# Kernel optimization log

Hardware: AMD Instinct MI355X
Metric: run time of the kernel (lower is better)

The kernel has to match this reference:

```python
import jax, jax.numpy as jnp
import numpy as np

NUM_USERS = 60000
NUM_ITEMS = 30000
EMBED_K = 64
FEAT_DIM = 64
E_HALF = 1000000
N_LAYERS = 3
LM = 0.5
BATCH = 100000
EPS = 1e-8


def setup_inputs() -> dict:
    key = jax.random.key(0)
    ks = jax.random.split(key, 14)
    Gu = jax.random.normal(ks[0], (NUM_USERS, EMBED_K), jnp.float32) * 0.05
    Gi = jax.random.normal(ks[1], (NUM_ITEMS, EMBED_K), jnp.float32) * 0.05
    Bu = jax.random.normal(ks[2], (NUM_USERS, 1), jnp.float32) * 0.05
    Bi = jax.random.normal(ks[3], (NUM_ITEMS, 1), jnp.float32) * 0.05
    Mu = jax.random.normal(ks[4], (1, 1), jnp.float32) * 0.05
    proj_W = jax.random.normal(ks[5], (FEAT_DIM, EMBED_K), jnp.float32) * 0.05
    proj_b = jnp.zeros((EMBED_K,), jnp.float32)
    gcn_W = jax.random.normal(ks[6], (N_LAYERS, EMBED_K, EMBED_K), jnp.float32) * 0.05
    gcn_b = jnp.zeros((N_LAYERS, EMBED_K), jnp.float32)
    edge_features = jax.random.normal(ks[7], (E_HALF, FEAT_DIM), jnp.float32)
    # first half rows MUST be item-node ids (>= NUM_USERS) since update_adjacency
    # indexes node_embeddings[row[:E//2] - num_users]
    users = jax.random.randint(ks[8], (E_HALF,), 0, NUM_USERS, jnp.int32)
    items = jax.random.randint(ks[9], (E_HALF,), 0, NUM_ITEMS, jnp.int32) + NUM_USERS
    edge_row = jnp.concatenate([items, users], axis=0)
    edge_col = jnp.concatenate([users, items], axis=0)
    L0 = jnp.ones((2 * E_HALF,), jnp.float32)
    user_idx = jax.random.randint(ks[10], (BATCH,), 0, NUM_USERS, jnp.int32)
    item_idx = jax.random.randint(ks[11], (BATCH,), 0, NUM_ITEMS, jnp.int32)
    return {"Gu": Gu, "Gi": Gi, "Bu": Bu, "Bi": Bi, "Mu": Mu,
            "proj_W": proj_W, "proj_b": proj_b, "gcn_W": gcn_W, "gcn_b": gcn_b,
            "edge_features": edge_features, "L0": L0,
            "edge_row": edge_row, "edge_col": edge_col,
            "user_idx": user_idx, "item_idx": item_idx}


def reference(Gu, Gi, Bu, Bi, Mu, proj_W, proj_b, gcn_W, gcn_b,
              edge_features, L0, edge_row, edge_col, user_idx, item_idx):
    num_users = Gu.shape[0]
    N = num_users + Gi.shape[0]
    Eh = edge_features.shape[0]
    row_h = edge_row[:Eh]  # item-node ids for the first (undirected) half
    # projection of edge features is identical every layer -> hoist
    proj = edge_features @ proj_W + proj_b  # [Eh, K]
    x = jnp.concatenate([Gu, Gi], axis=0)  # [N, K]
    for l in range(gcn_W.shape[0]):
        # update_adjacency (aggr='sim'): cosine sim of feature-gated endpoint embeddings
        rn = x[row_h]                       # [Eh, K] gather
        cn = x[row_h - num_users]           # [Eh, K] gather (as in original code)
        a = rn * proj
        b = cn * proj
        na = jnp.maximum(jnp.sqrt(jnp.sum(a * a, -1)), EPS)
        nb = jnp.maximum(jnp.sqrt(jnp.sum(b * b, -1)), EPS)
        sim = jax.nn.relu(jnp.sum(a * b, -1) / (na * nb))
        vals = LM * L0 + (1.0 - LM) * jnp.concatenate([sim, sim], axis=0)  # [E]
        # GCNConv with normalize=True, add_self_loops=False on weighted adjacency
        deg = jax.ops.segment_sum(vals, edge_row, num_segments=N)
        dinv = jnp.where(deg > 0, jax.lax.rsqrt(jnp.where(deg > 0, deg, 1.0)), 0.0)
        ew = dinv[edge_row] * vals * dinv[edge_col]   # [E]
        h = x @ gcn_W[l]                               # [N, K]
        agg = jax.ops.segment_sum(ew[:, None] * h[edge_col], edge_row, num_segments=N)
        x = jax.nn.relu(agg + gcn_b[l])
    gu = x[:num_users]
    gi = x[num_users:]
    # forward/predict: dot-product + biases + global offset
    xui = (jnp.sum(gu[user_idx] * gi[item_idx], axis=1)
           + Bu[user_idx, 0] + Bi[item_idx, 0] + Mu[0, 0])
    return xui
```

## Files before the change

kernel.cpp:

```cpp
#include <hip/hip_runtime.h>
#include <hip/hip_fp16.h>

#define NUSERS 60000
#define NITEMS 30000
#define NNODES 90000
#define KDIM 64
#define EH 1000000
#define E2 2000000
#define NBATCH 100000
#define EPSV 1e-8f

#define NB 128
#define RPB_I 240
#define RPB_U 472
#define CHUNK 2048
#define NPAD_I 32768
#define NPAD_U 61440

typedef __attribute__((ext_vector_type(8))) short short8v;
typedef __attribute__((ext_vector_type(4))) float f32x4;

__device__ inline float4 h4_to_f4(const __half* p) {
    float2 raw = *(const float2*)p;
    __half2 a = *(__half2*)&raw.x;
    __half2 b = *(__half2*)&raw.y;
    float2 fa = __half22float2(a), fb = __half22float2(b);
    return make_float4(fa.x, fa.y, fb.x, fb.y);
}

__global__ void k_count2(const int* __restrict__ erow, const int* __restrict__ ecol,
                         int* __restrict__ cntI, int* __restrict__ cntU) {
    int e = blockIdx.x * 256 + threadIdx.x;
    if (e < EH) {
        atomicAdd(&cntI[erow[e] - NUSERS], 1);
        atomicAdd(&cntU[ecol[e]], 1);
    }
}

__global__ void k_scan2(const int* __restrict__ cntI, int* __restrict__ ofsI,
                        int* __restrict__ curI, const int* __restrict__ cntU,
                        int* __restrict__ ofsU, int* __restrict__ curU) {
    const int* counts; int* offsets; int* cursor; int n;
    if (blockIdx.x == 0) { counts = cntI; offsets = ofsI; cursor = curI; n = NITEMS; }
    else                 { counts = cntU; offsets = ofsU; cursor = curU; n = NUSERS; }
    __shared__ int wsum[17];
    int t = threadIdx.x;
    int lane = t & 63, wid = t >> 6;
    int carry = 0;
    int npad = (n + 4095) & ~4095;
    for (int base = 0; base < npad; base += 4096) {
        int i0 = base + t * 4;
        int4 v = *(const int4*)&counts[i0];
        int s0 = v.x, s1 = s0 + v.y, s2 = s1 + v.z, s3 = s2 + v.w;
        int ws = s3;
#pragma unroll
        for (int o = 1; o < 64; o <<= 1) {
            int u = __shfl_up(ws, o, 64);
            if (lane >= o) ws += u;
        }
        if (lane == 63) wsum[wid] = ws;
        __syncthreads();
        if (wid == 0) {
            int wv = (lane < 16) ? wsum[lane] : 0;
#pragma unroll
            for (int o = 1; o < 16; o <<= 1) {
                int u = __shfl_up(wv, o, 64);
                if (lane >= o) wv += u;
            }
            if (lane < 16) wsum[lane] = wv;
            if (lane == 15) wsum[16] = wv;
        }
        __syncthreads();
        int wbase = (wid > 0) ? wsum[wid - 1] : 0;
        int texcl = carry + wbase + (ws - s3);
        if (i0 < n)     { offsets[i0]     = texcl;      cursor[i0]     = texcl; }
        if (i0 + 1 < n) { offsets[i0 + 1] = texcl + s0; cursor[i0 + 1] = texcl + s0; }
        if (i0 + 2 < n) { offsets[i0 + 2] = texcl + s1; cursor[i0 + 2] = texcl + s1; }
        if (i0 + 3 < n) { offsets[i0 + 3] = texcl + s2; cursor[i0 + 3] = texcl + s2; }
        carry += wsum[16];
        __syncthreads();
    }
    if (t == 0) offsets[n] = carry;
}

__global__ void k_bcur2(const int* __restrict__ ofsI, const int* __restrict__ ofsU,
                        int* __restrict__ gcurI, int* __restrict__ gcurU) {
    int t = threadIdx.x;
    if (t < NB) {
        int rI = t * RPB_I; if (rI > NITEMS) rI = NITEMS;
        int rU = t * RPB_U; if (rU > NUSERS) rU = NUSERS;
        gcurI[t] = ofsI[rI];
        gcurU[t] = ofsU[rU];
    }
}

template <int PHASE, int RPBX>
__global__ void k_binA(const int* __restrict__ erow, const int* __restrict__ ecol,
                       const int* __restrict__ inv, int* __restrict__ gcur,
                       int* __restrict__ srow, int2* __restrict__ spay) {
    __shared__ int bcnt[NB];
    __shared__ int bbase[NB];
    __shared__ int bpos[NB];
    __shared__ int bglob[NB];
    __shared__ int wtot[2];
    __shared__ int lrow[CHUNK];
    __shared__ int2 lce[CHUNK];
    int t = threadIdx.x;
    for (int base = blockIdx.x * CHUNK; base < EH; base += gridDim.x * CHUNK) {
        for (int i = t; i < NB; i += 256) bcnt[i] = 0;
        __syncthreads();
        int mr[8], mx[8], my[8], mb[8];
#pragma unroll
        for (int k = 0; k < 8; ++k) {
            int e = base + k * 256 + t;
            if (e < EH) {
                int r, px, py;
                if (PHASE == 0) { r = erow[e] - NUSERS; px = ecol[e]; py = e; }
                else            { r = ecol[e];          px = erow[e]; py = inv[e]; }
                mr[k] = r; mx[k] = px; my[k] = py;
                mb[k] = r / RPBX;
                atomicAdd(&bcnt[mb[k]], 1);
            } else {
                mb[k] = -1;
            }
        }
        __syncthreads();
        if (t < NB) {
            int v = bcnt[t];
            int s = v;
#pragma unroll
            for (int o = 1; o < 64; o <<= 1) {
                int u = __shfl_up(s, o, 64);
                if ((t & 63) >= o) s += u;
            }
            bbase[t] = s - v;
            if ((t & 63) == 63) wtot[t >> 6] = s;
        }
        __syncthreads();
        if (t >= 64 && t < NB) bbase[t] += wtot[0];
        if (t < NB) bpos[t] = 0;
        __syncthreads();
#pragma unroll
        for (int k = 0; k < 8; ++k) {
            if (mb[k] >= 0) {
                int p = bbase[mb[k]] + atomicAdd(&bpos[mb[k]], 1);
                lrow[p] = mr[k];
                lce[p] = make_int2(mx[k], my[k]);
            }
        }
        __syncthreads();
        if (t < NB) bglob[t] = bcnt[t] ? atomicAdd(&gcur[t], bcnt[t]) : 0;
        __syncthreads();
        int total = bbase[NB - 1] + bcnt[NB - 1];
        for (int i = t; i < total; i += 256) {
            int r = lrow[i];
            int b = r / RPBX;
            int dest = bglob[b] + (i - bbase[b]);
            srow[dest] = r;
            spay[dest] = lce[i];
        }
        __syncthreads();
    }
}

__global__ void k_binB0(const int* __restrict__ srow, const int2* __restrict__ spay,
                        const int* __restrict__ ofsI, int* __restrict__ curI,
                        const float* __restrict__ L0, int* __restrict__ colp,
                        int* __restrict__ eorig, int* __restrict__ inv,
                        float2* __restrict__ L0p) {
    int b = blockIdx.x;
    int r0 = b * RPB_I; if (r0 > NITEMS) r0 = NITEMS;
    int r1 = (b + 1) * RPB_I; if (r1 > NITEMS) r1 = NITEMS;
    int lo = ofsI[r0], hi = ofsI[r1];
    for (int i = lo + threadIdx.x; i < hi; i += blockDim.x) {
        int r = srow[i];
        int2 p = spay[i];
        int slot = atomicAdd(&curI[r], 1);
        colp[slot] = p.x;
        eorig[slot] = p.y;
        inv[p.y] = slot;
        L0p[slot] = make_float2(L0[p.y], L0[p.y + EH]);
    }
}

__global__ void k_binB1(const int* __restrict__ srow, const int2* __restrict__ spay,
                        const int* __restrict__ ofsU, int* __restrict__ curU,
                        int2* __restrict__ csrU) {
    int b = blockIdx.x;
    int r0 = b * RPB_U; if (r0 > NUSERS) r0 = NUSERS;
    int r1 = (b + 1) * RPB_U; if (r1 > NUSERS) r1 = NUSERS;
    int lo = ofsU[r0], hi = ofsU[r1];
    for (int i = lo + threadIdx.x; i < hi; i += blockDim.x) {
        int r = srow[i];
        int2 p = spay[i];
        int slot = atomicAdd(&curU[r], 1);
        csrU[slot] = p;
    }
}

template <int MODE>
__global__ void k_gemm(const float* __restrict__ A, const float* __restrict__ W,
                       const float* __restrict__ bias, void* __restrict__ out, int M,
                       const int* __restrict__ eorig, __half* __restrict__ xh) {
    __shared__ float Ws[4096];
    int t = threadIdx.x;
    for (int i = t; i < 4096; i += 256) Ws[i] = W[i];
    __syncthreads();
    int lane = t & 63;
    int wid = t >> 6;
    int lr = lane & 15;
    int kg = lane >> 4;
    short8v Bh[2][4], Bl[2][4];
#pragma unroll
    for (int kt = 0; kt < 2; ++kt)
#pragma unroll
        for (int ct = 0; ct < 4; ++ct) {
            short8v bh, bl;
#pragma unroll
            for (int i = 0; i < 8; ++i) {
                int k = kt * 32 + kg * 8 + i;
                float v = Ws[k * 64 + ct * 16 + lr];
                unsigned u = __float_as_uint(v);
                float d = v - __uint_as_float(u & 0xffff0000u);
                bh[i] = (short)(u >> 16);
                bl[i] = (short)(__float_as_uint(d) >> 16);
            }
            Bh[kt][ct] = bh;
            Bl[kt][ct] = bl;
        }
    float bcol[4];
    if (MODE == 1) {
#pragma unroll
        for (int ct = 0; ct < 4; ++ct) bcol[ct] = bias[ct * 16 + lr];
    }
    int nt = M >> 4;
    int nw = gridDim.x * 4;
    for (int tile = blockIdx.x * 4 + wid; tile < nt; tile += nw) {
        int r0 = tile << 4;
        int arow = (MODE == 1) ? eorig[r0 + lr] : (r0 + lr);
        const float* ap = &A[(size_t)arow * 64 + kg * 8];
        float4 a0 = *(const float4*)ap;
        float4 a1 = *(const float4*)(ap + 4);
        float4 a2 = *(const float4*)(ap + 32);
        float4 a3 = *(const float4*)(ap + 36);
        float av[16] = {a0.x, a0.y, a0.z, a0.w, a1.x, a1.y, a1.z, a1.w,
                        a2.x, a2.y, a2.z, a2.w, a3.x, a3.y, a3.z, a3.w};
        if (MODE == 0) {
            short8v pk0, pk1;
#pragma unroll
            for (int i = 0; i < 8; ++i) {
                pk0[i] = __half_as_short(__float2half(av[i]));
                pk1[i] = __half_as_short(__float2half(av[8 + i]));
            }
            *(short8v*)&xh[(size_t)(r0 + lr) * 64 + kg * 8] = pk0;
            *(short8v*)&xh[(size_t)(r0 + lr) * 64 + 32 + kg * 8] = pk1;
        }
        short8v Ah[2], Al[2];
#pragma unroll
        for (int kt = 0; kt < 2; ++kt) {
            short8v ah, al;
#pragma unroll
            for (int i = 0; i < 8; ++i) {
                float v = av[kt * 8 + i];
                unsigned u = __float_as_uint(v);
                float d = v - __uint_as_float(u & 0xffff0000u);
                ah[i] = (short)(u >> 16);
                al[i] = (short)(__float_as_uint(d) >> 16);
            }
            Ah[kt] = ah;
            Al[kt] = al;
        }
        f32x4 acc[4] = {{0, 0, 0, 0}, {0, 0, 0, 0}, {0, 0, 0, 0}, {0, 0, 0, 0}};
#pragma unroll
        for (int kt = 0; kt < 2; ++kt)
#pragma unroll
            for (int ct = 0; ct < 4; ++ct) {
                acc[ct] = __builtin_amdgcn_mfma_f32_16x16x32_bf16(Ah[kt], Bh[kt][ct], acc[ct], 0, 0, 0);
                acc[ct] = __builtin_amdgcn_mfma_f32_16x16x32_bf16(Al[kt], Bh[kt][ct], acc[ct], 0, 0, 0);
                acc[ct] = __builtin_amdgcn_mfma_f32_16x16x32_bf16(Ah[kt], Bl[kt][ct], acc[ct], 0, 0, 0);
            }
#pragma unroll
        for (int ct = 0; ct < 4; ++ct)
#pragma unroll
            for (int r = 0; r < 4; ++r) {
                int row = r0 + kg * 4 + r;
                int col = ct * 16 + lr;
                float p = acc[ct][r];
                if (MODE == 1) {
                    p += bcol[ct];
                    ((__half*)out)[(size_t)row * 64 + col] = __float2half(p * p);
                } else {
                    ((__half*)out)[(size_t)row * 64 + col] = __float2half(p);
                }
            }
    }
}

__global__ void __launch_bounds__(256) k_sim(
        const __half* __restrict__ xh, const __half* __restrict__ qp,
        const int* __restrict__ colp, const float2* __restrict__ L0p,
        const int* __restrict__ ofsI, float* __restrict__ v1p,
        float* __restrict__ v2p, float* __restrict__ deg) {
    int t = threadIdx.x;
    int wid = t >> 6, lane = t & 63, g = lane >> 4, kq = lane & 15;
    int item = blockIdx.x * 4 + wid;
    if (item >= NITEMS) return;
    float4 rn = h4_to_f4(&xh[(size_t)(NUSERS + item) * 64 + kq * 4]);
    int jb = ofsI[item], je = ofsI[item + 1];
    float dacc = 0.0f;
    for (int j0 = jb; j0 < je; j0 += 4) {
        int j = j0 + g;
        bool act = j < je;
        int user = 0;
        float4 cn = make_float4(0, 0, 0, 0), qv = make_float4(0, 0, 0, 0);
        if (act) {
            user = colp[j];
            cn = h4_to_f4(&xh[(size_t)user * 64 + kq * 4]);
            qv = h4_to_f4(&qp[(size_t)j * 64 + kq * 4]);
        }
        float aa = rn.x * rn.x * qv.x + rn.y * rn.y * qv.y + rn.z * rn.z * qv.z + rn.w * rn.w * qv.w;
        float bb = cn.x * cn.x * qv.x + cn.y * cn.y * qv.y + cn.z * cn.z * qv.z + cn.w * cn.w * qv.w;
        float ab = rn.x * cn.x * qv.x + rn.y * cn.y * qv.y + rn.z * cn.z * qv.z + rn.w * cn.w * qv.w;
#pragma unroll
        for (int m = 1; m < 16; m <<= 1) {
            aa += __shfl_xor(aa, m, 64);
            bb += __shfl_xor(bb, m, 64);
            ab += __shfl_xor(ab, m, 64);
        }
        if (kq == 0 && act) {
            float na = fmaxf(sqrtf(aa), EPSV);
            float nb = fmaxf(sqrtf(bb), EPSV);
            float sim = fmaxf(ab / (na * nb), 0.0f);
            float2 l0 = L0p[j];
            float v1 = 0.5f * l0.x + 0.5f * sim;
            float v2 = 0.5f * l0.y + 0.5f * sim;
            v1p[j] = v1;
            v2p[j] = v2;
            atomicAdd(&deg[user], v2);
            dacc += v1;
        }
    }
    dacc += __shfl_xor(dacc, 16, 64);
    dacc += __shfl_xor(dacc, 32, 64);
    if (lane == 0) deg[NUSERS + item] = dacc;
}

__global__ void k_dinv(const float* __restrict__ deg, float* __restrict__ dinv) {
    int n = blockIdx.x * 256 + threadIdx.x;
    if (n < NNODES) {
        float d = deg[n];
        dinv[n] = d > 0.0f ? rsqrtf(d) : 0.0f;
    }
}

#define IBLK 3750
__global__ void __launch_bounds__(256) k_agg(
        const int* __restrict__ ofsI, const int* __restrict__ colp,
        const float* __restrict__ v1p, const int* __restrict__ ofsU,
        const int2* __restrict__ csrU, const float* __restrict__ v2p,
        const float* __restrict__ dinv, const __half* __restrict__ h,
        const float* __restrict__ bias, float* __restrict__ xo) {
    int t = threadIdx.x;
    int half_id = t >> 5, sl = t & 31;
    const __half2* h2 = (const __half2*)h;
    float2 bv = ((const float2*)bias)[sl];
    float2 acc = make_float2(0.0f, 0.0f);
    int node;
    if (blockIdx.x < IBLK) {
        int il = blockIdx.x * 8 + half_id;
        node = NUSERS + il;
        float dn = dinv[node];
        int jb = ofsI[il], je = ofsI[il + 1];
        for (int j0 = jb; j0 < je; j0 += 32) {
            int cnt = je - j0;
            if (cnt > 32) cnt = 32;
            int col = 0;
            float wgt = 0.0f;
            if (sl < cnt) {
                col = colp[j0 + sl];
                wgt = dn * v1p[j0 + sl] * dinv[col];
            }
            for (int u = 0; u < cnt; ++u) {
                int c = __shfl(col, u, 32);
                float wv = __shfl(wgt, u, 32);
                float2 hv = __half22float2(h2[(size_t)c * 32 + sl]);
                acc.x += wv * hv.x;
                acc.y += wv * hv.y;
            }
        }
    } else {
        int ul = (blockIdx.x - IBLK) * 8 + half_id;
        node = ul;
        float dn = dinv[ul];
        int jb = ofsU[ul], je = ofsU[ul + 1];
        for (int j0 = jb; j0 < je; j0 += 32) {
            int cnt = je - j0;
            if (cnt > 32) cnt = 32;
            int col = 0;
            float wgt = 0.0f;
            if (sl < cnt) {
                int2 ce = csrU[j0 + sl];
                col = ce.x;
                wgt = dn * v2p[ce.y] * dinv[col];
            }
            for (int u = 0; u < cnt; ++u) {
                int c = __shfl(col, u, 32);
                float wv = __shfl(wgt, u, 32);
                float2 hv = __half22float2(h2[(size_t)c * 32 + sl]);
                acc.x += wv * hv.x;
                acc.y += wv * hv.y;
            }
        }
    }
    float2 o = make_float2(fmaxf(acc.x + bv.x, 0.0f), fmaxf(acc.y + bv.y, 0.0f));
    ((float2*)xo)[(size_t)node * 32 + sl] = o;
}

__global__ void k_final(const float* __restrict__ x, const int* __restrict__ uidx,
                        const int* __restrict__ iidx, const float* __restrict__ Bu,
                        const float* __restrict__ Bi, const float* __restrict__ Mu,
                        float* __restrict__ out) {
    int t = threadIdx.x;
    int le = t >> 4, kq = t & 15, k0 = kq * 4;
    int i = blockIdx.x * 16 + le;
    if (i >= NBATCH) return;
    int u = uidx[i], it = iidx[i];
    float4 a = *(const float4*)&x[(size_t)u * 64 + k0];
    float4 b = *(const float4*)&x[(size_t)(NUSERS + it) * 64 + k0];
    float d = a.x * b.x + a.y * b.y + a.z * b.z + a.w * b.w;
#pragma unroll
    for (int m = 1; m < 16; m <<= 1) d += __shfl_xor(d, m, 64);
    if (kq == 0) out[i] = d + Bu[u] + Bi[it] + Mu[0];
}

extern "C" void kernel_launch(void* const* d_in, const int* in_sizes, int n_in,
                              void* d_out, int out_size, void* d_ws, size_t ws_size,
                              hipStream_t stream) {
    const float* Gu    = (const float*)d_in[0];
    const float* Gi    = (const float*)d_in[1];
    const float* Bu    = (const float*)d_in[2];
    const float* Bi    = (const float*)d_in[3];
    const float* Mu    = (const float*)d_in[4];
    const float* projW = (const float*)d_in[5];
    const float* projb = (const float*)d_in[6];
    const float* gcnW  = (const float*)d_in[7];
    const float* gcnb  = (const float*)d_in[8];
    const float* ef    = (const float*)d_in[9];
    const float* L0    = (const float*)d_in[10];
    const int*   erow  = (const int*)d_in[11];
    const int*   ecol  = (const int*)d_in[12];
    const int*   uidx  = (const int*)d_in[13];
    const int*   iidx  = (const int*)d_in[14];
    float* out = (float*)d_out;

    char* w = (char*)d_ws;
    size_t off = 0;
    auto take = [&](size_t bytes) -> void* {
        void* p = w + off;
        off += (bytes + 255) & ~(size_t)255;
        return p;
    };
    float*  x0    = (float*)take((size_t)NNODES * KDIM * 4);
    float*  x1    = (float*)take((size_t)NNODES * KDIM * 4);
    __half* h     = (__half*)take((size_t)NNODES * KDIM * 2);
    __half* xh    = (__half*)take((size_t)NNODES * KDIM * 2);
    float*  v1p   = (float*)take((size_t)EH * 4);
    float*  v2p   = (float*)take((size_t)EH * 4);
    float*  deg   = (float*)take((size_t)NNODES * 4);
    float*  dinv  = (float*)take((size_t)NNODES * 4);
    int*    cntI  = (int*)take((size_t)NPAD_I * 4);
    int*    cntU  = (int*)take((size_t)NPAD_U * 4);
    int*    ofsI  = (int*)take((size_t)(NITEMS + 1) * 4);
    int*    curI  = (int*)take((size_t)(NITEMS + 1) * 4);
    int*    ofsU  = (int*)take((size_t)(NUSERS + 1) * 4);
    int*    curU  = (int*)take((size_t)(NUSERS + 1) * 4);
    int*    gcurI = (int*)take((size_t)NB * 4);
    int*    gcurU = (int*)take((size_t)NB * 4);
    int*    colp  = (int*)take((size_t)EH * 4);
    int*    eorig = (int*)take((size_t)EH * 4);
    int*    inv   = (int*)take((size_t)EH * 4);
    float2* L0p   = (float2*)take((size_t)EH * 8);
    int2*   csrU  = (int2*)take((size_t)EH * 8);
    __half* qp    = (__half*)take((size_t)EH * KDIM * 2);
    int*  srow = (int*)qp;
    int2* spay = (int2*)((char*)qp + (size_t)EH * 4);

    hipMemsetAsync(cntI, 0, (size_t)(NPAD_I + NPAD_U) * 4, stream);
    k_count2<<<(EH + 255) / 256, 256, 0, stream>>>(erow, ecol, cntI, cntU);
    k_scan2<<<2, 1024, 0, stream>>>(cntI, ofsI, curI, cntU, ofsU, curU);
    k_bcur2<<<1, 128, 0, stream>>>(ofsI, ofsU, gcurI, gcurU);
    k_binA<0, RPB_I><<<256, 256, 0, stream>>>(erow, ecol, nullptr, gcurI, srow, spay);
    k_binB0<<<NB, 512, 0, stream>>>(srow, spay, ofsI, curI, L0, colp, eorig, inv, L0p);
    k_binA<1, RPB_U><<<256, 256, 0, stream>>>(erow, ecol, inv, gcurU, srow, spay);
    k_binB1<<<NB, 512, 0, stream>>>(srow, spay, ofsU, curU, csrU);

    k_gemm<1><<<1024, 256, 0, stream>>>(ef, projW, projb, qp, EH, eorig, nullptr);

    hipMemcpyAsync(x0, Gu, (size_t)NUSERS * KDIM * 4, hipMemcpyDeviceToDevice, stream);
    hipMemcpyAsync(x0 + (size_t)NUSERS * KDIM, Gi, (size_t)NITEMS * KDIM * 4,
                   hipMemcpyDeviceToDevice, stream);

    float* xc = x0;
    float* xn = x1;
    for (int l = 0; l < 3; ++l) {
        k_gemm<0><<<512, 256, 0, stream>>>(xc, gcnW + (size_t)l * 4096, nullptr, h,
                                           NNODES, nullptr, xh);
        hipMemsetAsync(deg, 0, (size_t)NUSERS * 4, stream);
        k_sim<<<(NITEMS + 3) / 4, 256, 0, stream>>>(xh, qp, colp, L0p, ofsI, v1p, v2p, deg);
        k_dinv<<<(NNODES + 255) / 256, 256, 0, stream>>>(deg, dinv);
        k_agg<<<IBLK + NUSERS / 8, 256, 0, stream>>>(ofsI, colp, v1p, ofsU, csrU, v2p,
                                                     dinv, h, gcnb + (size_t)l * 64, xn);
        float* tswap = xc; xc = xn; xn = tswap;
    }
    k_final<<<(NBATCH + 15) / 16, 256, 0, stream>>>(xc, uidx, iidx, Bu, Bi, Mu, out);
}
```

Before: 897.8 us.

## Reorder GCN layer to aggregate before weight GEMM and keep node features in fp16

Uses linearity of aggregation to gather raw fp16 node features first and apply the weight matrix, bias and ReLU afterwards in a fused GEMM epilogue. The fp32 x ping-pong buffers and the separate per-layer fp16 conversion go away, along with the device memcpy of the initial embeddings. Degree zeroing moves into the aggregation kernel, so a per-layer memset disappears. The aggregated result is rounded to fp16 before the GEMM, which adds some precision risk.

```diff
diff --git a/kernel.cpp b/kernel.cpp
--- a/kernel.cpp
+++ b/kernel.cpp
@@ -199,9 +199,9 @@
 }
 
 template <int MODE>
-__global__ void k_gemm(const float* __restrict__ A, const float* __restrict__ W,
-                       const float* __restrict__ bias, void* __restrict__ out, int M,
-                       const int* __restrict__ eorig, __half* __restrict__ xh) {
+__global__ void k_gemm(const void* __restrict__ Ap, const float* __restrict__ W,
+                       const float* __restrict__ bias, __half* __restrict__ out,
+                       int M, const int* __restrict__ eorig) {
     __shared__ float Ws[4096];
     int t = threadIdx.x;
     for (int i = t; i < 4096; i += 256) Ws[i] = W[i];
@@ -229,31 +229,33 @@
             Bl[kt][ct] = bl;
         }
     float bcol[4];
-    if (MODE == 1) {
-#pragma unroll
-        for (int ct = 0; ct < 4; ++ct) bcol[ct] = bias[ct * 16 + lr];
-    }
+#pragma unroll
+    for (int ct = 0; ct < 4; ++ct) bcol[ct] = bias[ct * 16 + lr];
     int nt = M >> 4;
     int nw = gridDim.x * 4;
     for (int tile = blockIdx.x * 4 + wid; tile < nt; tile += nw) {
         int r0 = tile << 4;
-        int arow = (MODE == 1) ? eorig[r0 + lr] : (r0 + lr);
-        const float* ap = &A[(size_t)arow * 64 + kg * 8];
-        float4 a0 = *(const float4*)ap;
-        float4 a1 = *(const float4*)(ap + 4);
-        float4 a2 = *(const float4*)(ap + 32);
-        float4 a3 = *(const float4*)(ap + 36);
-        float av[16] = {a0.x, a0.y, a0.z, a0.w, a1.x, a1.y, a1.z, a1.w,
-                        a2.x, a2.y, a2.z, a2.w, a3.x, a3.y, a3.z, a3.w};
-        if (MODE == 0) {
-            short8v pk0, pk1;
+        float av[16];
+        if (MODE == 1) {
+            int arow = eorig[r0 + lr];
+            const float* ap = &((const float*)Ap)[(size_t)arow * 64 + kg * 8];
+            float4 a0 = *(const float4*)ap;
+            float4 a1 = *(const float4*)(ap + 4);
+            float4 a2 = *(const float4*)(ap + 32);
+            float4 a3 = *(const float4*)(ap + 36);
+            av[0]=a0.x; av[1]=a0.y; av[2]=a0.z; av[3]=a0.w;
+            av[4]=a1.x; av[5]=a1.y; av[6]=a1.z; av[7]=a1.w;
+            av[8]=a2.x; av[9]=a2.y; av[10]=a2.z; av[11]=a2.w;
+            av[12]=a3.x; av[13]=a3.y; av[14]=a3.z; av[15]=a3.w;
+        } else {
+            const ushort* ap = &((const ushort*)Ap)[(size_t)(r0 + lr) * 64 + kg * 8];
+            short8v a01 = *(const short8v*)ap;
+            short8v a23 = *(const short8v*)(ap + 32);
 #pragma unroll
             for (int i = 0; i < 8; ++i) {
-                pk0[i] = __half_as_short(__float2half(av[i]));
-                pk1[i] = __half_as_short(__float2half(av[8 + i]));
-            }
-            *(short8v*)&xh[(size_t)(r0 + lr) * 64 + kg * 8] = pk0;
-            *(short8v*)&xh[(size_t)(r0 + lr) * 64 + 32 + kg * 8] = pk1;
+                av[i]     = __half2float(__ushort_as_half((ushort)a01[i]));
+                av[8 + i] = __half2float(__ushort_as_half((ushort)a23[i]));
+            }
         }
         short8v Ah[2], Al[2];
 #pragma unroll
@@ -285,12 +287,11 @@
             for (int r = 0; r < 4; ++r) {
                 int row = r0 + kg * 4 + r;
                 int col = ct * 16 + lr;
-                float p = acc[ct][r];
+                float p = acc[ct][r] + bcol[ct];
                 if (MODE == 1) {
-                    p += bcol[ct];
-                    ((__half*)out)[(size_t)row * 64 + col] = __float2half(p * p);
+                    out[(size_t)row * 64 + col] = __float2half(p * p);
                 } else {
-                    ((__half*)out)[(size_t)row * 64 + col] = __float2half(p);
+                    out[(size_t)row * 64 + col] = __float2half(fmaxf(p, 0.0f));
                 }
             }
     }
@@ -358,12 +359,11 @@
         const int* __restrict__ ofsI, const int* __restrict__ colp,
         const float* __restrict__ v1p, const int* __restrict__ ofsU,
         const int2* __restrict__ csrU, const float* __restrict__ v2p,
-        const float* __restrict__ dinv, const __half* __restrict__ h,
-        const float* __restrict__ bias, float* __restrict__ xo) {
+        const float* __restrict__ dinv, const __half* __restrict__ xh,
+        __half* __restrict__ agg, float* __restrict__ deg) {
     int t = threadIdx.x;
     int half_id = t >> 5, sl = t & 31;
-    const __half2* h2 = (const __half2*)h;
-    float2 bv = ((const float2*)bias)[sl];
+    const __half2* h2 = (const __half2*)xh;
     float2 acc = make_float2(0.0f, 0.0f);
     int node;
     if (blockIdx.x < IBLK) {
@@ -412,11 +412,22 @@
             }
         }
     }
-    float2 o = make_float2(fmaxf(acc.x + bv.x, 0.0f), fmaxf(acc.y + bv.y, 0.0f));
-    ((float2*)xo)[(size_t)node * 32 + sl] = o;
-}
-
-__global__ void k_final(const float* __restrict__ x, const int* __restrict__ uidx,
+    if (sl == 0) deg[node] = 0.0f;
+    ((__half2*)agg)[(size_t)node * 32 + sl] = __floats2half2_rn(acc.x, acc.y);
+}
+
+__global__ void k_cvt0(const float* __restrict__ Gu, const float* __restrict__ Gi,
+                       __half* __restrict__ xh) {
+    int i = blockIdx.x * 256 + threadIdx.x;
+    int idx = i * 4;
+    if (idx >= NNODES * KDIM) return;
+    const float* src = idx < NUSERS * KDIM ? &Gu[idx] : &Gi[idx - NUSERS * KDIM];
+    float4 v = *(const float4*)src;
+    ((__half2*)xh)[idx / 2]     = __floats2half2_rn(v.x, v.y);
+    ((__half2*)xh)[idx / 2 + 1] = __floats2half2_rn(v.z, v.w);
+}
+
+__global__ void k_final(const __half* __restrict__ xh, const int* __restrict__ uidx,
                         const int* __restrict__ iidx, const float* __restrict__ Bu,
                         const float* __restrict__ Bi, const float* __restrict__ Mu,
                         float* __restrict__ out) {
@@ -425,8 +436,8 @@
     int i = blockIdx.x * 16 + le;
     if (i >= NBATCH) return;
     int u = uidx[i], it = iidx[i];
-    float4 a = *(const float4*)&x[(size_t)u * 64 + k0];
-    float4 b = *(const float4*)&x[(size_t)(NUSERS + it) * 64 + k0];
+    float4 a = h4_to_f4(&xh[(size_t)u * 64 + k0]);
+    float4 b = h4_to_f4(&xh[(size_t)(NUSERS + it) * 64 + k0]);
     float d = a.x * b.x + a.y * b.y + a.z * b.z + a.w * b.w;
 #pragma unroll
     for (int m = 1; m < 16; m <<= 1) d += __shfl_xor(d, m, 64);
@@ -460,10 +471,8 @@
         off += (bytes + 255) & ~(size_t)255;
         return p;
     };
-    float*  x0    = (float*)take((size_t)NNODES * KDIM * 4);
-    float*  x1    = (float*)take((size_t)NNODES * KDIM * 4);
-    __half* h     = (__half*)take((size_t)NNODES * KDIM * 2);
     __half* xh    = (__half*)take((size_t)NNODES * KDIM * 2);
+    __half* agg   = (__half*)take((size_t)NNODES * KDIM * 2);
     float*  v1p   = (float*)take((size_t)EH * 4);
     float*  v2p   = (float*)take((size_t)EH * 4);
     float*  deg   = (float*)take((size_t)NNODES * 4);
@@ -494,23 +503,18 @@
     k_binA<1, RPB_U><<<256, 256, 0, stream>>>(erow, ecol, inv, gcurU, srow, spay);
     k_binB1<<<NB, 512, 0, stream>>>(srow, spay, ofsU, curU, csrU);
 
-    k_gemm<1><<<1024, 256, 0, stream>>>(ef, projW, projb, qp, EH, eorig, nullptr);
-
-    hipMemcpyAsync(x0, Gu, (size_t)NUSERS * KDIM * 4, hipMemcpyDeviceToDevice, stream);
-    hipMemcpyAsync(x0 + (size_t)NUSERS * KDIM, Gi, (size_t)NITEMS * KDIM * 4,
-                   hipMemcpyDeviceToDevice, stream);
-
-    float* xc = x0;
-    float* xn = x1;
+    k_gemm<1><<<1024, 256, 0, stream>>>(ef, projW, projb, qp, EH, eorig);
+
+    k_cvt0<<<(NNODES * KDIM / 4 + 255) / 256, 256, 0, stream>>>(Gu, Gi, xh);
+    hipMemsetAsync(deg, 0, (size_t)NNODES * 4, stream);
+
     for (int l = 0; l < 3; ++l) {
-        k_gemm<0><<<512, 256, 0, stream>>>(xc, gcnW + (size_t)l * 4096, nullptr, h,
-                                           NNODES, nullptr, xh);
-        hipMemsetAsync(deg, 0, (size_t)NUSERS * 4, stream);
         k_sim<<<(NITEMS + 3) / 4, 256, 0, stream>>>(xh, qp, colp, L0p, ofsI, v1p, v2p, deg);
         k_dinv<<<(NNODES + 255) / 256, 256, 0, stream>>>(deg, dinv);
         k_agg<<<IBLK + NUSERS / 8, 256, 0, stream>>>(ofsI, colp, v1p, ofsU, csrU, v2p,
-                                                     dinv, h, gcnb + (size_t)l * 64, xn);
-        float* tswap = xc; xc = xn; xn = tswap;
-    }
-    k_final<<<(NBATCH + 15) / 16, 256, 0, stream>>>(xc, uidx, iidx, Bu, Bi, Mu, out);
-}
+                                                     dinv, xh, agg, deg);
+        k_gemm<2><<<512, 256, 0, stream>>>(agg, gcnW + (size_t)l * 4096,
+                                           gcnb + (size_t)l * 64, xh, NNODES, nullptr);
+    }
+    k_final<<<(NBATCH + 15) / 16, 256, 0, stream>>>(xh, uidx, iidx, Bu, Bi, Mu, out);
+}
```

After: 878.5 us. 2.2% less time.
